# Kernel optimization log

Hardware: AMD Instinct MI355X
Metric: run time of the kernel (lower is better)

Reference implementation:

```python
import jax, jax.numpy as jnp
import numpy as np

N = 50000
E = 800000
D = 128
DOUT = 128
KEEP_SCALE = 2.0  # 1 / (1 - drop_rate), drop_rate = 0.5


def setup_inputs() -> dict:
    key = jax.random.key(0)
    k1, k2, k3, k4, k5, k6 = jax.random.split(key, 6)
    X = jax.random.normal(k1, (N, D), dtype=jnp.float32)
    W = jax.random.normal(k2, (2 * D, DOUT), dtype=jnp.float32) * (1.0 / np.sqrt(2 * D))
    b = jax.random.normal(k3, (DOUT,), dtype=jnp.float32) * 0.01
    src = jax.random.randint(k4, (E,), 0, N, dtype=jnp.int32)
    dst = jax.random.randint(k5, (E,), 0, N, dtype=jnp.int32)
    drop_mask = jax.random.randint(k6, (N, DOUT), 0, 2, dtype=jnp.int32)
    return {"X": X, "W": W, "b": b, "src": src, "dst": dst, "drop_mask": drop_mask}


def reference(X, W, b, src, dst, drop_mask):
    # v2v mean aggregation: X_nbr[i] = mean_{(j->i) in E} X[j]
    nbr_sum = jax.ops.segment_sum(X[src], dst, num_segments=N)        # [N, D]
    deg = jax.ops.segment_sum(jnp.ones((E,), X.dtype), dst, num_segments=N)  # [N]
    X_nbr = nbr_sum / jnp.maximum(deg, 1.0)[:, None]
    # concat + linear + relu + dropout (deterministic mask, train-mode scaling)
    H = jnp.concatenate([X, X_nbr], axis=1)                           # [N, 2D]
    out = jax.nn.relu(H @ W + b)
    out = out * (drop_mask.astype(out.dtype) * KEEP_SCALE)
    return out
```

## Files before the change

### kernel.cpp

```cpp
#include <hip/hip_runtime.h>

#define NN 50000
#define ND 50048
#define NW 6256
#define NE 800000
#define CHUNKS 32
#define EPC 25000
#define CAP 56
#define NTILE 3125
#define CVT_UNITS 1600000
#define CVT_BLOCKS 1563

typedef __attribute__((ext_vector_type(8))) short short8;
typedef __attribute__((ext_vector_type(4))) float f32x4;
typedef __attribute__((ext_vector_type(2))) float f32x2;
typedef __attribute__((ext_vector_type(4))) unsigned int u32x4;
typedef __attribute__((ext_vector_type(2))) unsigned int u32x2;


__device__ __forceinline__ unsigned f2bf(float f) {
  unsigned u = __builtin_bit_cast(unsigned, f);
  return (u + 0x7fffu + ((u >> 16) & 1u)) >> 16;
}

#if defined(__has_builtin) && __has_builtin(__builtin_amdgcn_cvt_pk_fp8_f32) && \
    __has_builtin(__builtin_amdgcn_cvt_pk_f32_fp8)
#define FP8_HW 1
#else
#define FP8_HW 0
#endif

#if !FP8_HW
__device__ __forceinline__ unsigned f2fp8(float x) {
  unsigned u = __builtin_bit_cast(unsigned, x);
  unsigned s = (u >> 24) & 0x80u;
  float a = __builtin_bit_cast(float, u & 0x7fffffffu);
  if (a < 0.015625f) {
    unsigned q = (unsigned)(a * 512.0f + 0.5f);
    return s | (q == 8u ? 0x08u : q);
  }
  if (a >= 448.0f) return s | 0x7Eu;
  unsigned v = u & 0x7fffffffu;
  v = v + 0x0007FFFFu + ((v >> 20) & 1u);
  unsigned e = (v >> 23) - 120u;
  if (e >= 16u) return s | 0x7Eu;
  return s | (e << 3) | ((v >> 20) & 7u);
}
__device__ __forceinline__ float fp82f(unsigned b) {
  unsigned s = (b & 0x80u) << 24;
  unsigned e = (b >> 3) & 15u;
  unsigned m = b & 7u;
  unsigned mag = e ? ((e + 120u) << 23) | (m << 20)
                   : __builtin_bit_cast(unsigned, (float)m * 0.001953125f);
  return __builtin_bit_cast(float, s | mag);
}
#endif

__global__ __launch_bounds__(1024) void k_rankconv(const int* __restrict__ dst,
                                                   const float* __restrict__ W,
                                                   const float* __restrict__ X,
                                                   unsigned char* __restrict__ rank,
                                                   unsigned int* __restrict__ chunkcnt,
                                                   u32x4* __restrict__ Wfrag,
                                                   u32x2* __restrict__ Xbf2,
                                                   unsigned int* __restrict__ Xf8w) {
  int tid = threadIdx.x;
  int c = blockIdx.x;
  if (c >= CHUNKS) {
    int i = (c - CHUNKS) * 1024 + tid;
    if (i < CVT_UNITS) {
      f32x4 v = ((const f32x4*)X)[i];
      u32x2 o;
      o[0] = f2bf(v[0]) | (f2bf(v[1]) << 16);
      o[1] = f2bf(v[2]) | (f2bf(v[3]) << 16);
      Xbf2[i] = o;
      unsigned p8;
#if FP8_HW
      p8 = __builtin_amdgcn_cvt_pk_fp8_f32(v[0], v[1], 0, false);
      p8 = __builtin_amdgcn_cvt_pk_fp8_f32(v[2], v[3], p8, true);
#else
      p8 = f2fp8(v[0]) | (f2fp8(v[1]) << 8) | (f2fp8(v[2]) << 16) | (f2fp8(v[3]) << 24);
#endif
      Xf8w[i] = p8;
    } else if (i < CVT_UNITS + 32) {
      Xbf2[i] = (u32x2){0u, 0u};
      Xf8w[i] = 0u;
    }
    return;
  }
  __shared__ unsigned int pack[NW];
  if (tid < 128) {
    int s = c * 128 + tid;
    int lane = s & 63;
    int t = (s >> 6) & 7;
    int kb = s >> 9;
    int col = t * 16 + (lane & 15);
    int k0 = kb * 32 + (lane >> 4) * 8;
    u32x4 o;
#pragma unroll
    for (int p = 0; p < 4; ++p) {
      unsigned lo = f2bf(W[(k0 + 2 * p) * 128 + col]);
      unsigned hi = f2bf(W[(k0 + 2 * p + 1) * 128 + col]);
      o[p] = lo | (hi << 16);
    }
    Wfrag[s] = o;
  }
  for (int w = tid; w < NW; w += 1024) pack[w] = 0;
  __syncthreads();
  int ebase = c * EPC;
  for (int i = tid; i < EPC; i += 1024) {
    int e = ebase + i;
    int d = dst[e];
    unsigned sh = (unsigned)(d & 7) * 4u;
    unsigned old = atomicAdd(&pack[d >> 3], 1u << sh);
    rank[e] = (unsigned char)((old >> sh) & 15u);
  }
  __syncthreads();
  for (int w = tid; w < NW; w += 1024) chunkcnt[(size_t)c * NW + w] = pack[w];
}

__global__ __launch_bounds__(64) void k_base(const unsigned int* __restrict__ chunkcnt,
                                             unsigned char* __restrict__ chunkbase,
                                             unsigned int* __restrict__ deg) {
  int d = blockIdx.x * 64 + threadIdx.x;
  if (d >= NN) return;
  int w = d >> 3;
  unsigned sh = (unsigned)(d & 7) * 4u;
  unsigned cnts[CHUNKS];
#pragma unroll
  for (int c = 0; c < CHUNKS; ++c) cnts[c] = chunkcnt[(size_t)c * NW + w];
  unsigned run = 0;
#pragma unroll
  for (int c = 0; c < CHUNKS; ++c) {
    chunkbase[(size_t)c * ND + d] = (unsigned char)run;
    run += (cnts[c] >> sh) & 15u;
  }
  deg[d] = run;
}

__global__ __launch_bounds__(256) void k_place(const int* __restrict__ src,
                                               const int* __restrict__ dst,
                                               const unsigned char* __restrict__ rank,
                                               const unsigned char* __restrict__ chunkbase,
                                               unsigned short* __restrict__ slots) {
  int e = blockIdx.x * 256 + threadIdx.x;
  if (e >= NE) return;
  int c = e / EPC;
  int d = dst[e];
  int pos = (int)chunkbase[(size_t)c * ND + d] + (int)rank[e];
  if (pos < CAP) slots[d * CAP + pos] = (unsigned short)src[e];
}

__global__ __launch_bounds__(256) void k_fused(const unsigned short* __restrict__ Xbf,
                                               const unsigned char* __restrict__ Xf8,
                                               const unsigned int* __restrict__ deg,
                                               const unsigned short* __restrict__ slots,
                                               const u32x4* __restrict__ Wfrag,
                                               const float* __restrict__ b,
                                               const int* __restrict__ mask,
                                               float* __restrict__ out) {
  __shared__ unsigned short nbr[16 * 136];
  int lane = threadIdx.x & 63;
  int wid = threadIdx.x >> 6;
  int tile = blockIdx.x;
  int gl = lane >> 4;
  int ill = lane & 15;
  int q = lane >> 3;
  int il8 = lane & 7;
  int g2 = q >> 1;
  int p = q & 1;
  const u32x4* Xb4 = (const u32x4*)Xbf;
  const u32x4* X84 = (const u32x4*)Xf8;
  int t0 = wid * 2;
  int t1 = wid * 2 + 1;

  int node_l = tile * 16 + wid * 4 + gl;
  const unsigned short* sl = slots + node_l * CAP;
  int s0 = sl[ill];
  int s1 = sl[16 + ill];
  int s2 = sl[32 + ill];
  int s3 = sl[min(48 + ill, CAP - 1)];

  int node = tile * 16 + wid * 4 + g2;
  int dg = (int)deg[node];
  int m = min(dg, CAP);
  int mmax = m;
  mmax = max(mmax, __shfl_xor(mmax, 8, 64));
  mmax = max(mmax, __shfl_xor(mmax, 16, 64));
  mmax = max(mmax, __shfl_xor(mmax, 32, 64));
  float acc[16];
#pragma unroll
  for (int k = 0; k < 16; ++k) acc[k] = 0.f;

#define SLOT2(e)                                                             \
  ({                                                                         \
    int t_ = __shfl((e) < 16 ? s0 : (e) < 32 ? s1 : (e) < 48 ? s2 : s3,      \
                    g2 * 16 + ((e) & 15), 64);                               \
    ((e) < m) ? t_ : NN;                                                     \
  })
#define LOAD1(v, bb)                            \
  {                                             \
    int e_ = 2 * (bb) + p;                      \
    int r_ = SLOT2(e_);                         \
    v = X84[(size_t)r_ * 8 + il8];              \
  }
#if FP8_HW
#define ACC16(v)                                                        \
  {                                                                     \
    _Pragma("unroll") for (int w_ = 0; w_ < 4; ++w_) {                  \
      f32x2 lo_ = __builtin_amdgcn_cvt_pk_f32_fp8((int)v[w_], false);   \
      f32x2 hi_ = __builtin_amdgcn_cvt_pk_f32_fp8((int)v[w_], true);    \
      acc[4 * w_ + 0] += lo_[0];                                        \
      acc[4 * w_ + 1] += lo_[1];                                        \
      acc[4 * w_ + 2] += hi_[0];                                        \
      acc[4 * w_ + 3] += hi_[1];                                        \
    }                                                                   \
  }
#else
#define ACC16(v)                                                        \
  {                                                                     \
    _Pragma("unroll") for (int w_ = 0; w_ < 4; ++w_) {                  \
      unsigned b_ = v[w_];                                              \
      acc[4 * w_ + 0] += fp82f(b_ & 255u);                              \
      acc[4 * w_ + 1] += fp82f((b_ >> 8) & 255u);                       \
      acc[4 * w_ + 2] += fp82f((b_ >> 16) & 255u);                      \
      acc[4 * w_ + 3] += fp82f(b_ >> 24);                               \
    }                                                                   \
  }
#endif

  int nbb = (mmax + 1) >> 1;
  u32x4 p0, p1, p2, p3;
  LOAD1(p0, 0)
  LOAD1(p1, 1)

  int mk0[4], mk1[4];
#pragma unroll
  for (int rg = 0; rg < 4; ++rg) {
    mk0[rg] = mask[(size_t)(tile * 16 + gl * 4 + rg) * 128 + t0 * 16 + ill];
    mk1[rg] = mask[(size_t)(tile * 16 + gl * 4 + rg) * 128 + t1 * 16 + ill];
  }
  float b0 = b[t0 * 16 + ill];
  float b1 = b[t1 * 16 + ill];

  LOAD1(p2, 2)
  LOAD1(p3, 3)

  int bb = 0;
  for (; bb + 4 <= nbb; bb += 4) {
    ACC16(p0) LOAD1(p0, bb + 4)
    ACC16(p1) LOAD1(p1, bb + 5)
    ACC16(p2) LOAD1(p2, bb + 6)
    ACC16(p3) LOAD1(p3, bb + 7)
  }
  if (bb < nbb) { ACC16(p0) ++bb; }
  if (bb < nbb) { ACC16(p1) ++bb; }
  if (bb < nbb) { ACC16(p2) ++bb; }
  if (bb < nbb) { ACC16(p3) ++bb; }
#undef SLOT2
#undef LOAD1
#undef ACC16

#pragma unroll
  for (int k = 0; k < 16; ++k) acc[k] += __shfl_xor(acc[k], 8, 64);

  if (p == 0) {
    float inv = 1.0f / (float)max(dg, 1);
    int r = wid * 4 + g2;
    u32x4 o0, o1;
#pragma unroll
    for (int pp = 0; pp < 4; ++pp) {
      o0[pp] = f2bf(acc[2 * pp] * inv) | (f2bf(acc[2 * pp + 1] * inv) << 16);
      o1[pp] = f2bf(acc[8 + 2 * pp] * inv) | (f2bf(acc[9 + 2 * pp] * inv) << 16);
    }
    *(u32x4*)(&nbr[r * 136 + il8 * 16]) = o0;
    *(u32x4*)(&nbr[r * 136 + il8 * 16 + 8]) = o1;
  }
  __syncthreads();

  int arow = tile * 16 + ill;
  f32x4 c0 = (f32x4){0.f, 0.f, 0.f, 0.f};
  f32x4 c1 = (f32x4){0.f, 0.f, 0.f, 0.f};
#pragma unroll
  for (int kb = 0; kb < 4; ++kb) {
    short8 a = __builtin_bit_cast(short8, Xb4[(size_t)arow * 16 + kb * 4 + gl]);
    short8 w0 = __builtin_bit_cast(short8, Wfrag[(kb * 8 + t0) * 64 + lane]);
    short8 w1 = __builtin_bit_cast(short8, Wfrag[(kb * 8 + t1) * 64 + lane]);
    c0 = __builtin_amdgcn_mfma_f32_16x16x32_bf16(a, w0, c0, 0, 0, 0);
    c1 = __builtin_amdgcn_mfma_f32_16x16x32_bf16(a, w1, c1, 0, 0, 0);
  }
#pragma unroll
  for (int kb = 0; kb < 4; ++kb) {
    short8 a = *(const short8*)(&nbr[ill * 136 + kb * 32 + gl * 8]);
    short8 w0 = __builtin_bit_cast(short8, Wfrag[((kb + 4) * 8 + t0) * 64 + lane]);
    short8 w1 = __builtin_bit_cast(short8, Wfrag[((kb + 4) * 8 + t1) * 64 + lane]);
    c0 = __builtin_amdgcn_mfma_f32_16x16x32_bf16(a, w0, c0, 0, 0, 0);
    c1 = __builtin_amdgcn_mfma_f32_16x16x32_bf16(a, w1, c1, 0, 0, 0);
  }

  int orow = tile * 16 + gl * 4;
#pragma unroll
  for (int rg = 0; rg < 4; ++rg) {
    size_t i0 = (size_t)(orow + rg) * 128 + t0 * 16 + ill;
    size_t i1 = (size_t)(orow + rg) * 128 + t1 * 16 + ill;
    out[i0] = fmaxf(c0[rg] + b0, 0.f) * (2.0f * (float)mk0[rg]);
    out[i1] = fmaxf(c1[rg] + b1, 0.f) * (2.0f * (float)mk1[rg]);
  }
}

extern "C" void kernel_launch(void* const* d_in, const int* in_sizes, int n_in,
                              void* d_out, int out_size, void* d_ws, size_t ws_size,
                              hipStream_t stream) {
  (void)in_sizes; (void)n_in; (void)out_size; (void)ws_size;
  const float* X = (const float*)d_in[0];
  const float* W = (const float*)d_in[1];
  const float* b = (const float*)d_in[2];
  const int* src = (const int*)d_in[3];
  const int* dst = (const int*)d_in[4];
  const int* mask = (const int*)d_in[5];
  float* out = (float*)d_out;

  char* ws = (char*)d_ws;
  u32x4* Wfrag = (u32x4*)ws;
  unsigned int* deg = (unsigned int*)(ws + 65536);
  unsigned short* slots = (unsigned short*)(ws + 265728);
  unsigned int* Xf8w = (unsigned int*)(ws + 5865728);
  const unsigned char* Xf8 = (const unsigned char*)(ws + 5865728);
  u32x2* Xbf2 = (u32x2*)(ws + 12265984);
  const unsigned short* Xbf = (const unsigned short*)(ws + 12265984);
  unsigned char* rank = (unsigned char*)(ws + 25066240);
  unsigned int* chunkcnt = (unsigned int*)(ws + 25866240);
  unsigned char* chunkbase = (unsigned char*)(ws + 26667008);

  k_rankconv<<<CHUNKS + CVT_BLOCKS, 1024, 0, stream>>>(dst, W, X, rank, chunkcnt, Wfrag,
                                                       Xbf2, Xf8w);
  k_base<<<(NN + 63) / 64, 64, 0, stream>>>(chunkcnt, chunkbase, deg);
  k_place<<<(NE + 255) / 256, 256, 0, stream>>>(src, dst, rank, chunkbase, slots);
  k_fused<<<NTILE, 256, 0, stream>>>(Xbf, Xf8, deg, slots, Wfrag, b, mask, out);
}
```

Before: 67.92 us.

## Split fp8 features into two column planes and overlap gather with self MFMA

Stores the fp8 copy of X as two 64-column planes so each gather load covers half a row. The aggregation is restructured so each wave processes one node per 16-lane group, with four edge slots per group, and runs one plane after the other. The self-feature MFMA is moved between gather issue and accumulate to hide gather latency. Nontemporal loads and stores are added for streaming data. This changes how rows are fetched and adds extra shuffle reductions, with some risk of lower memory-level parallelism per lane.

```diff
diff --git a/kernel.cpp b/kernel.cpp
--- a/kernel.cpp
+++ b/kernel.cpp
@@ -10,6 +10,8 @@
 #define NTILE 3125
 #define CVT_UNITS 1600000
 #define CVT_BLOCKS 1563
+#define PLANEB 3200064
+#define PLANE32 800016
 
 typedef __attribute__((ext_vector_type(8))) short short8;
 typedef __attribute__((ext_vector_type(4))) float f32x4;
@@ -68,8 +70,9 @@
   int c = blockIdx.x;
   if (c >= CHUNKS) {
     int i = (c - CHUNKS) * 1024 + tid;
-    if (i < CVT_UNITS) {
-      f32x4 v = ((const f32x4*)X)[i];
+    if (i < CVT_UNITS + 32) {
+      f32x4 v = (f32x4){0.f, 0.f, 0.f, 0.f};
+      if (i < CVT_UNITS) v = ((const f32x4*)X)[i];
       u32x2 o;
       o[0] = f2bf(v[0]) | (f2bf(v[1]) << 16);
       o[1] = f2bf(v[2]) | (f2bf(v[3]) << 16);
@@ -81,10 +84,9 @@
 #else
       p8 = f2fp8(v[0]) | (f2fp8(v[1]) << 8) | (f2fp8(v[2]) << 16) | (f2fp8(v[3]) << 24);
 #endif
-      Xf8w[i] = p8;
-    } else if (i < CVT_UNITS + 32) {
-      Xbf2[i] = (u32x2){0u, 0u};
-      Xf8w[i] = 0u;
+      int r = i >> 5;
+      int d0 = (i & 31) * 4;
+      Xf8w[(d0 >> 6) * PLANE32 + r * 16 + ((d0 & 63) >> 2)] = p8;
     }
     return;
   }
@@ -165,44 +167,50 @@
   int tile = blockIdx.x;
   int gl = lane >> 4;
   int ill = lane & 15;
-  int q = lane >> 3;
-  int il8 = lane & 7;
-  int g2 = q >> 1;
-  int p = q & 1;
+  int es = (lane >> 2) & 3;
+  int il4 = lane & 3;
   const u32x4* Xb4 = (const u32x4*)Xbf;
-  const u32x4* X84 = (const u32x4*)Xf8;
-  int t0 = wid * 2;
-  int t1 = wid * 2 + 1;
-
-  int node_l = tile * 16 + wid * 4 + gl;
-  const unsigned short* sl = slots + node_l * CAP;
-  int s0 = sl[ill];
-  int s1 = sl[16 + ill];
-  int s2 = sl[32 + ill];
-  int s3 = sl[min(48 + ill, CAP - 1)];
-
-  int node = tile * 16 + wid * 4 + g2;
+  int t0c = wid * 2, t1c = wid * 2 + 1;
+
+  int node = tile * 16 + wid * 4 + gl;
+  const unsigned short* sl = slots + node * CAP;
+  int s0 = __builtin_nontemporal_load(sl + ill);
+  int s1 = __builtin_nontemporal_load(sl + 16 + ill);
+  int s2 = __builtin_nontemporal_load(sl + 32 + ill);
+  int s3 = __builtin_nontemporal_load(sl + min(48 + ill, CAP - 1));
   int dg = (int)deg[node];
   int m = min(dg, CAP);
   int mmax = m;
-  mmax = max(mmax, __shfl_xor(mmax, 8, 64));
   mmax = max(mmax, __shfl_xor(mmax, 16, 64));
   mmax = max(mmax, __shfl_xor(mmax, 32, 64));
+
+  int arow = tile * 16 + ill;
+  u32x4 aself[4];
+#pragma unroll
+  for (int kb = 0; kb < 4; ++kb)
+    aself[kb] = __builtin_nontemporal_load(Xb4 + (size_t)arow * 16 + kb * 4 + gl);
+  int mk0[4], mk1[4];
+#pragma unroll
+  for (int rg = 0; rg < 4; ++rg) {
+    mk0[rg] = __builtin_nontemporal_load(mask + (size_t)(tile * 16 + gl * 4 + rg) * 128 + t0c * 16 + ill);
+    mk1[rg] = __builtin_nontemporal_load(mask + (size_t)(tile * 16 + gl * 4 + rg) * 128 + t1c * 16 + ill);
+  }
+  float b0 = b[t0c * 16 + ill];
+  float b1 = b[t1c * 16 + ill];
+
+  const u32x4* P0 = (const u32x4*)Xf8;
+  const u32x4* P1 = (const u32x4*)(Xf8 + PLANEB);
   float acc[16];
-#pragma unroll
-  for (int k = 0; k < 16; ++k) acc[k] = 0.f;
-
-#define SLOT2(e)                                                             \
-  ({                                                                         \
-    int t_ = __shfl((e) < 16 ? s0 : (e) < 32 ? s1 : (e) < 48 ? s2 : s3,      \
-                    g2 * 16 + ((e) & 15), 64);                               \
-    ((e) < m) ? t_ : NN;                                                     \
-  })
-#define LOAD1(v, bb)                            \
-  {                                             \
-    int e_ = 2 * (bb) + p;                      \
-    int r_ = SLOT2(e_);                         \
-    v = X84[(size_t)r_ * 8 + il8];              \
+  f32x4 c0 = (f32x4){0.f, 0.f, 0.f, 0.f};
+  f32x4 c1 = (f32x4){0.f, 0.f, 0.f, 0.f};
+
+#define SREG(t) ((t) < 4 ? s0 : (t) < 8 ? s1 : (t) < 12 ? s2 : s3)
+#define GLOAD(vv, t, P)                                       \
+  if ((t) * 4 < mmax) {                                       \
+    int e_ = 4 * (t) + es;                                    \
+    int r_ = __shfl(SREG(t), gl * 16 + (e_ & 15), 64);        \
+    r_ = (e_ < m) ? r_ : NN;                                  \
+    vv = P[(size_t)r_ * 4 + il4];                             \
   }
 #if FP8_HW
 #define ACC16(v)                                                        \
@@ -228,72 +236,91 @@
     }                                                                   \
   }
 #endif
-
-  int nbb = (mmax + 1) >> 1;
-  u32x4 p0, p1, p2, p3;
-  LOAD1(p0, 0)
-  LOAD1(p1, 1)
-
-  int mk0[4], mk1[4];
-#pragma unroll
-  for (int rg = 0; rg < 4; ++rg) {
-    mk0[rg] = mask[(size_t)(tile * 16 + gl * 4 + rg) * 128 + t0 * 16 + ill];
-    mk1[rg] = mask[(size_t)(tile * 16 + gl * 4 + rg) * 128 + t1 * 16 + ill];
-  }
-  float b0 = b[t0 * 16 + ill];
-  float b1 = b[t1 * 16 + ill];
-
-  LOAD1(p2, 2)
-  LOAD1(p3, 3)
-
-  int bb = 0;
-  for (; bb + 4 <= nbb; bb += 4) {
-    ACC16(p0) LOAD1(p0, bb + 4)
-    ACC16(p1) LOAD1(p1, bb + 5)
-    ACC16(p2) LOAD1(p2, bb + 6)
-    ACC16(p3) LOAD1(p3, bb + 7)
-  }
-  if (bb < nbb) { ACC16(p0) ++bb; }
-  if (bb < nbb) { ACC16(p1) ++bb; }
-  if (bb < nbb) { ACC16(p2) ++bb; }
-  if (bb < nbb) { ACC16(p3) ++bb; }
-#undef SLOT2
-#undef LOAD1
-#undef ACC16
-
-#pragma unroll
-  for (int k = 0; k < 16; ++k) acc[k] += __shfl_xor(acc[k], 8, 64);
-
-  if (p == 0) {
-    float inv = 1.0f / (float)max(dg, 1);
-    int r = wid * 4 + g2;
-    u32x4 o0, o1;
-#pragma unroll
-    for (int pp = 0; pp < 4; ++pp) {
-      o0[pp] = f2bf(acc[2 * pp] * inv) | (f2bf(acc[2 * pp + 1] * inv) << 16);
-      o1[pp] = f2bf(acc[8 + 2 * pp] * inv) | (f2bf(acc[9 + 2 * pp] * inv) << 16);
-    }
-    *(u32x4*)(&nbr[r * 136 + il8 * 16]) = o0;
-    *(u32x4*)(&nbr[r * 136 + il8 * 16 + 8]) = o1;
-  }
-  __syncthreads();
-
-  int arow = tile * 16 + ill;
-  f32x4 c0 = (f32x4){0.f, 0.f, 0.f, 0.f};
-  f32x4 c1 = (f32x4){0.f, 0.f, 0.f, 0.f};
+#define GACC(vv, t)                                           \
+  if ((t) * 4 < mmax) { ACC16(vv) }
+#define COMBINE_WRITE(p)                                                      \
+  {                                                                           \
+    _Pragma("unroll") for (int k = 0; k < 16; ++k)                            \
+        acc[k] += __shfl_xor(acc[k], 4, 64);                                  \
+    _Pragma("unroll") for (int k = 0; k < 16; ++k)                            \
+        acc[k] += __shfl_xor(acc[k], 8, 64);                                  \
+    if (es == 0) {                                                            \
+      float inv = 1.0f / (float)max(dg, 1);                                   \
+      int r_ = wid * 4 + gl;                                                  \
+      u32x4 w0v, w1v;                                                         \
+      _Pragma("unroll") for (int pp = 0; pp < 4; ++pp) {                      \
+        w0v[pp] = f2bf(acc[2 * pp] * inv) | (f2bf(acc[2 * pp + 1] * inv) << 16); \
+        w1v[pp] = f2bf(acc[8 + 2 * pp] * inv) | (f2bf(acc[9 + 2 * pp] * inv) << 16); \
+      }                                                                       \
+      unsigned short* bp = &nbr[r_ * 136 + (p) * 64 + il4 * 16];              \
+      *(u32x4*)bp = w0v;                                                      \
+      *(u32x4*)(bp + 8) = w1v;                                                \
+    }                                                                         \
+  }
+
+#pragma unroll
+  for (int k = 0; k < 16; ++k) acc[k] = 0.f;
+  u32x4 v0, v1, v2, v3;
+  GLOAD(v0, 0, P0) GLOAD(v1, 1, P0) GLOAD(v2, 2, P0) GLOAD(v3, 3, P0)
+
 #pragma unroll
   for (int kb = 0; kb < 4; ++kb) {
-    short8 a = __builtin_bit_cast(short8, Xb4[(size_t)arow * 16 + kb * 4 + gl]);
-    short8 w0 = __builtin_bit_cast(short8, Wfrag[(kb * 8 + t0) * 64 + lane]);
-    short8 w1 = __builtin_bit_cast(short8, Wfrag[(kb * 8 + t1) * 64 + lane]);
+    short8 a = __builtin_bit_cast(short8, aself[kb]);
+    short8 w0 = __builtin_bit_cast(short8, Wfrag[(kb * 8 + t0c) * 64 + lane]);
+    short8 w1 = __builtin_bit_cast(short8, Wfrag[(kb * 8 + t1c) * 64 + lane]);
     c0 = __builtin_amdgcn_mfma_f32_16x16x32_bf16(a, w0, c0, 0, 0, 0);
     c1 = __builtin_amdgcn_mfma_f32_16x16x32_bf16(a, w1, c1, 0, 0, 0);
   }
+
+  GACC(v0, 0)  GLOAD(v0, 4, P0)
+  GACC(v1, 1)  GLOAD(v1, 5, P0)
+  GACC(v2, 2)  GLOAD(v2, 6, P0)
+  GACC(v3, 3)  GLOAD(v3, 7, P0)
+  GACC(v0, 4)  GLOAD(v0, 8, P0)
+  GACC(v1, 5)  GLOAD(v1, 9, P0)
+  GACC(v2, 6)  GLOAD(v2, 10, P0)
+  GACC(v3, 7)  GLOAD(v3, 11, P0)
+  GACC(v0, 8)  GLOAD(v0, 12, P0)
+  GACC(v1, 9)  GLOAD(v1, 13, P0)
+  GACC(v2, 10)
+  GACC(v3, 11)
+  GACC(v0, 12)
+  GACC(v1, 13)
+  {
+    u32x4 n0, n1, n2, n3;
+    GLOAD(n0, 0, P1) GLOAD(n1, 1, P1) GLOAD(n2, 2, P1) GLOAD(n3, 3, P1)
+    COMBINE_WRITE(0)
+#pragma unroll
+    for (int k = 0; k < 16; ++k) acc[k] = 0.f;
+    GACC(n0, 0)  GLOAD(n0, 4, P1)
+    GACC(n1, 1)  GLOAD(n1, 5, P1)
+    GACC(n2, 2)  GLOAD(n2, 6, P1)
+    GACC(n3, 3)  GLOAD(n3, 7, P1)
+    GACC(n0, 4)  GLOAD(n0, 8, P1)
+    GACC(n1, 5)  GLOAD(n1, 9, P1)
+    GACC(n2, 6)  GLOAD(n2, 10, P1)
+    GACC(n3, 7)  GLOAD(n3, 11, P1)
+    GACC(n0, 8)  GLOAD(n0, 12, P1)
+    GACC(n1, 9)  GLOAD(n1, 13, P1)
+    GACC(n2, 10)
+    GACC(n3, 11)
+    GACC(n0, 12)
+    GACC(n1, 13)
+    COMBINE_WRITE(1)
+  }
+#undef SREG
+#undef GLOAD
+#undef GACC
+#undef ACC16
+#undef COMBINE_WRITE
+
+  __syncthreads();
+
 #pragma unroll
   for (int kb = 0; kb < 4; ++kb) {
     short8 a = *(const short8*)(&nbr[ill * 136 + kb * 32 + gl * 8]);
-    short8 w0 = __builtin_bit_cast(short8, Wfrag[((kb + 4) * 8 + t0) * 64 + lane]);
-    short8 w1 = __builtin_bit_cast(short8, Wfrag[((kb + 4) * 8 + t1) * 64 + lane]);
+    short8 w0 = __builtin_bit_cast(short8, Wfrag[((kb + 4) * 8 + t0c) * 64 + lane]);
+    short8 w1 = __builtin_bit_cast(short8, Wfrag[((kb + 4) * 8 + t1c) * 64 + lane]);
     c0 = __builtin_amdgcn_mfma_f32_16x16x32_bf16(a, w0, c0, 0, 0, 0);
     c1 = __builtin_amdgcn_mfma_f32_16x16x32_bf16(a, w1, c1, 0, 0, 0);
   }
@@ -301,10 +328,12 @@
   int orow = tile * 16 + gl * 4;
 #pragma unroll
   for (int rg = 0; rg < 4; ++rg) {
-    size_t i0 = (size_t)(orow + rg) * 128 + t0 * 16 + ill;
-    size_t i1 = (size_t)(orow + rg) * 128 + t1 * 16 + ill;
-    out[i0] = fmaxf(c0[rg] + b0, 0.f) * (2.0f * (float)mk0[rg]);
-    out[i1] = fmaxf(c1[rg] + b1, 0.f) * (2.0f * (float)mk1[rg]);
+    size_t i0 = (size_t)(orow + rg) * 128 + t0c * 16 + ill;
+    size_t i1 = (size_t)(orow + rg) * 128 + t1c * 16 + ill;
+    float o0 = fmaxf(c0[rg] + b0, 0.f) * (2.0f * (float)mk0[rg]);
+    float o1 = fmaxf(c1[rg] + b1, 0.f) * (2.0f * (float)mk1[rg]);
+    __builtin_nontemporal_store(o0, out + i0);
+    __builtin_nontemporal_store(o1, out + i1);
   }
 }
 
```

Measured after the change: 77.41 us. 14.0% more time.
